# Kernel optimization log

Measured on AMD Instinct MI355X. Metric: run time of the kernel, lower is better.

The kernel has to match this reference:

```python
import jax, jax.numpy as jnp
import numpy as np

V, H, F, E, S, N, O = 50000, 1024, 4096, 8, 128, 4096, 2


def setup_inputs() -> dict:
    key = jax.random.key(0)
    ks = jax.random.split(key, 9)
    x = jax.random.randint(ks[0], (N, S), 0, V)
    emb = jax.random.normal(ks[1], (V, H), dtype=jnp.float32) * 0.02
    emb = emb.at[0].set(0.0)  # padding_idx=0
    Wg = jax.random.normal(ks[2], (H, E), dtype=jnp.float32) * 0.02
    W1 = jax.random.normal(ks[3], (E, H, F), dtype=jnp.float32) * 0.02
    b1 = jnp.zeros((E, F), dtype=jnp.float32)
    W2 = jax.random.normal(ks[4], (E, F, H), dtype=jnp.float32) * 0.02
    b2 = jnp.zeros((E, H), dtype=jnp.float32)
    Wfc = jax.random.normal(ks[5], (H, O), dtype=jnp.float32) * 0.02
    bfc = jnp.zeros((O,), dtype=jnp.float32)
    return {"x": x, "emb": emb, "Wg": Wg, "W1": W1, "b1": b1,
            "W2": W2, "b2": b2, "Wfc": Wfc, "bfc": bfc}


def reference(x, emb, Wg, W1, b1, W2, b2, Wfc, bfc):
    # embedding lookup + mean pool over sequence: [N, S, H] -> [N, H]
    h = emb[x].mean(axis=1)
    # top-1 gating (deepspeed MoE default k=1)
    gates = jax.nn.softmax(h @ Wg, axis=-1)              # [N, E]
    idx = jnp.argmax(gates, axis=-1)                      # [N]
    onehot = jax.nn.one_hot(idx, E, dtype=h.dtype)        # [N, E]
    combine = gates * onehot                              # [N, E] top-1 prob
    # dense-dispatch reference for grouped expert GEMMs (FFN: H->F->H, ReLU)
    h1 = jax.nn.relu(jnp.einsum('nh,ehf->nef', h, W1) + b1)  # [N, E, F]
    h2 = jnp.einsum('nef,efh->neh', h1, W2) + b2             # [N, E, H]
    moe = jnp.einsum('ne,neh->nh', combine, h2)              # [N, H]
    return jax.nn.log_softmax(moe @ Wfc + bfc, axis=1)       # [N, O]
```

## Files before the change

kernel.cpp:

```cpp
#include <hip/hip_runtime.h>
#include <stdint.h>

#define V_SZ 50000
#define H_DIM 1024
#define F_DIM 4096
#define E_NUM 8
#define S_LEN 128
#define N_TOK 4096
#define NPAD (N_TOK + E_NUM*128)
#define EMB_SCALE 16.0f

typedef unsigned short u16;
typedef unsigned int u32;
typedef unsigned char u8;
typedef short bf16x8 __attribute__((ext_vector_type(8)));
typedef float f32x4 __attribute__((ext_vector_type(4)));
typedef float f32x2 __attribute__((ext_vector_type(2)));

__device__ __forceinline__ u16 f2bf(float f) {
  u32 u = __builtin_bit_cast(u32, f);
  u += 0x7fffu + ((u >> 16) & 1u);
  return (u16)(u >> 16);
}
__device__ __forceinline__ u32 pack2(float a, float b) {
  return (u32)f2bf(a) | ((u32)f2bf(b) << 16);
}

__device__ __forceinline__ void gld_lds16(u16* lds, const u16* g) {
  __builtin_amdgcn_global_load_lds((const __attribute__((address_space(1))) void*)g,
                                   (__attribute__((address_space(3))) void*)lds,
                                   16, 0, 0);
}

__global__ void embconv_kernel(const float* __restrict__ emb, u8* __restrict__ embf8) {
  const size_t total = (size_t)V_SZ*H_DIM/8;
  const size_t stride = (size_t)gridDim.x*blockDim.x;
  for (size_t i = (size_t)blockIdx.x*blockDim.x + threadIdx.x; i < total; i += stride) {
    const float4 a = ((const float4*)emb)[i*2];
    const float4 b = ((const float4*)emb)[i*2+1];
    u32 w0, w1;
    w0 = __builtin_amdgcn_cvt_pk_fp8_f32(a.x*EMB_SCALE, a.y*EMB_SCALE, 0u, false);
    w0 = __builtin_amdgcn_cvt_pk_fp8_f32(a.z*EMB_SCALE, a.w*EMB_SCALE, w0, true);
    w1 = __builtin_amdgcn_cvt_pk_fp8_f32(b.x*EMB_SCALE, b.y*EMB_SCALE, 0u, false);
    w1 = __builtin_amdgcn_cvt_pk_fp8_f32(b.z*EMB_SCALE, b.w*EMB_SCALE, w1, true);
    ((uint2*)embf8)[i] = make_uint2(w0, w1);
  }
}

__global__ void poolgate_kernel(const int* __restrict__ x, const u8* __restrict__ embf8,
                                const float* __restrict__ Wg,
                                u16* __restrict__ hB, float* __restrict__ gate_val,
                                int* __restrict__ gate_idx, int* __restrict__ cnt) {
  __shared__ int sidx[S_LEN];
  __shared__ float wsum[4][8];
  const int n = blockIdx.x, t = threadIdx.x;
  if (t < S_LEN) sidx[t] = x[n*S_LEN + t];
  __syncthreads();
  float a0 = 0.f, a1 = 0.f, a2 = 0.f, a3 = 0.f;
  #pragma unroll 8
  for (int s = 0; s < S_LEN; ++s) {
    const u32 w = *(const u32*)(embf8 + (size_t)sidx[s]*H_DIM + t*4);
    const f32x2 lo = __builtin_amdgcn_cvt_pk_f32_fp8(w, false);
    const f32x2 hi = __builtin_amdgcn_cvt_pk_f32_fp8(w, true);
    a0 += lo[0]; a1 += lo[1]; a2 += hi[0]; a3 += hi[1];
  }
  const float sc = 1.0f/((float)S_LEN * EMB_SCALE);
  a0 *= sc; a1 *= sc; a2 *= sc; a3 *= sc;
  uint2 pk; pk.x = pack2(a0, a1); pk.y = pack2(a2, a3);
  *(uint2*)&hB[(size_t)n*H_DIM + t*4] = pk;
  float lg[E_NUM];
  #pragma unroll
  for (int e = 0; e < E_NUM; ++e) lg[e] = 0.f;
  const float hv[4] = {a0, a1, a2, a3};
  #pragma unroll
  for (int j = 0; j < 4; ++j) {
    const float4* w4 = (const float4*)(Wg + (size_t)(t*4+j)*E_NUM);
    const float4 wa = w4[0], wb = w4[1];
    lg[0] += hv[j]*wa.x; lg[1] += hv[j]*wa.y; lg[2] += hv[j]*wa.z; lg[3] += hv[j]*wa.w;
    lg[4] += hv[j]*wb.x; lg[5] += hv[j]*wb.y; lg[6] += hv[j]*wb.z; lg[7] += hv[j]*wb.w;
  }
  #pragma unroll
  for (int m = 32; m >= 1; m >>= 1) {
    #pragma unroll
    for (int e = 0; e < E_NUM; ++e) lg[e] += __shfl_xor(lg[e], m);
  }
  if ((t & 63) == 0) {
    #pragma unroll
    for (int e = 0; e < E_NUM; ++e) wsum[t >> 6][e] = lg[e];
  }
  __syncthreads();
  if (t == 0) {
    float l[E_NUM];
    #pragma unroll
    for (int e = 0; e < E_NUM; ++e)
      l[e] = wsum[0][e] + wsum[1][e] + wsum[2][e] + wsum[3][e];
    float mx = l[0]; int im = 0;
    #pragma unroll
    for (int e = 1; e < E_NUM; ++e) if (l[e] > mx) { mx = l[e]; im = e; }
    float s = 0.f;
    #pragma unroll
    for (int e = 0; e < E_NUM; ++e) s += expf(l[e] - mx);
    gate_val[n] = 1.0f / s;
    gate_idx[n] = im;
    atomicAdd(&cnt[im], 1);
  }
}

__global__ void offsets_kernel(const int* __restrict__ cnt, int* __restrict__ pad_off) {
  int o = 0;
  for (int e = 0; e < E_NUM; ++e) {
    pad_off[e] = o;
    o += ((cnt[e] + 127) >> 7) << 7;
  }
  pad_off[E_NUM] = o;
}

__global__ void scatterconv_kernel(const u16* __restrict__ hB, const int* __restrict__ gate_idx,
                                   const int* __restrict__ pad_off, int* __restrict__ cursor,
                                   int* __restrict__ perm, u16* __restrict__ Hg) {
  __shared__ int srow;
  const int n = blockIdx.x, t = threadIdx.x;
  if (t == 0) {
    const int e = gate_idx[n];
    const int pos = atomicAdd(&cursor[e], 1);
    const int row = pad_off[e] + pos;
    perm[row] = n;
    srow = row;
  }
  __syncthreads();
  const int row = srow;
  const uint4 v = *(const uint4*)(hB + (size_t)n*H_DIM + t*8);
  *(uint4*)&Hg[(size_t)row*H_DIM + t*8] = v;
}

template<int C, int RPER>
__global__ void ct_kernel(const float* __restrict__ in, u16* __restrict__ out) {
  __shared__ float tile[64][65];
  const int c0 = blockIdx.x*64, r0 = blockIdx.y*64;
  const int t = threadIdx.x;
  const int cq = t & 15, rr = t >> 4;
  #pragma unroll
  for (int p = 0; p < 4; ++p) {
    const int row = p*16 + rr;
    float4 v = ((const float4*)(in + (size_t)(r0+row)*C + c0))[cq];
    tile[row][cq*4+0] = v.x; tile[row][cq*4+1] = v.y;
    tile[row][cq*4+2] = v.z; tile[row][cq*4+3] = v.w;
  }
  __syncthreads();
  const int slot = t & 7, nn = t >> 3;
  const int e = r0 / RPER, rl0 = r0 % RPER;
  u16* outE = out + (size_t)e*C*RPER;
  #pragma unroll
  for (int p = 0; p < 2; ++p) {
    const int nc = p*32 + nn;
    uint4 q;
    q.x = pack2(tile[slot*8+0][nc], tile[slot*8+1][nc]);
    q.y = pack2(tile[slot*8+2][nc], tile[slot*8+3][nc]);
    q.z = pack2(tile[slot*8+4][nc], tile[slot*8+5][nc]);
    q.w = pack2(tile[slot*8+6][nc], tile[slot*8+7][nc]);
    *(uint4*)&outE[(size_t)(c0+nc)*RPER + rl0 + slot*8] = q;
  }
}

template<int KTOT, int EPI>
__launch_bounds__(256, 2)
__global__ void gemm_kernel(const u16* __restrict__ A, const u16* __restrict__ B,
                            const float* __restrict__ bias,
                            const float* __restrict__ gate_val,
                            const int* __restrict__ perm,
                            const int* __restrict__ pad_off,
                            const int* __restrict__ cnt,
                            u16* __restrict__ out_bf, float* __restrict__ out_f) {
  constexpr int MD = (EPI == 1) ? F_DIM : H_DIM;
  const int e = blockIdx.z;
  const int seg0 = pad_off[e], seg1 = pad_off[e+1];
  if ((int)blockIdx.y*128 >= seg1 - seg0) return;
  const int t0 = seg0 + blockIdx.y*128;
  const int f0 = blockIdx.x*128;
  const u16* Ae = A + (size_t)e*MD*KTOT;

  __shared__ u16 As[128*64];
  __shared__ u16 Bs[128*64];

  const int tid = threadIdx.x;
  const int lane = tid & 63, wave = tid >> 6;
  const int wm = wave >> 1, wn = wave & 1;

  f32x4 acc[4][4];
  #pragma unroll
  for (int i = 0; i < 4; ++i)
    #pragma unroll
    for (int j = 0; j < 4; ++j) acc[i][j] = (f32x4){0.f, 0.f, 0.f, 0.f};

  const int rsub = lane >> 3, slot = lane & 7;
  const int csw = slot ^ rsub;
  const int fr = lane & 15, fg = lane >> 4;

  for (int kk = 0; kk < KTOT; kk += 64) {
    __syncthreads();
    #pragma unroll
    for (int i = 0; i < 4; ++i) {
      const int chunk = wave*4 + i;
      const int r = chunk*8 + rsub;
      gld_lds16(&As[chunk*512], Ae + (size_t)(f0 + r)*KTOT + kk + csw*8);
      gld_lds16(&Bs[chunk*512], B  + (size_t)(t0 + r)*KTOT + kk + csw*8);
    }
    __syncthreads();
    #pragma unroll
    for (int kh = 0; kh < 2; ++kh) {
      bf16x8 av[4], bv[4];
      #pragma unroll
      for (int mi = 0; mi < 4; ++mi) {
        const int ra = wm*64 + mi*16 + fr;
        const int sa = (kh*4 + fg) ^ (ra & 7);
        av[mi] = *(const bf16x8*)&As[ra*64 + sa*8];
      }
      #pragma unroll
      for (int ni = 0; ni < 4; ++ni) {
        const int rb = wn*64 + ni*16 + fr;
        const int sb = (kh*4 + fg) ^ (rb & 7);
        bv[ni] = *(const bf16x8*)&Bs[rb*64 + sb*8];
      }
      #pragma unroll
      for (int mi = 0; mi < 4; ++mi)
        #pragma unroll
        for (int ni = 0; ni < 4; ++ni)
          acc[mi][ni] = __builtin_amdgcn_mfma_f32_16x16x32_bf16(av[mi], bv[ni], acc[mi][ni], 0, 0, 0);
    }
  }

  #pragma unroll
  for (int mi = 0; mi < 4; ++mi) {
    const int gm0 = f0 + wm*64 + mi*16 + fg*4;
    #pragma unroll
    for (int ni = 0; ni < 4; ++ni) {
      const int gn = wn*64 + ni*16 + fr;
      if constexpr (EPI == 1) {
        const float* bp = bias + (size_t)e*MD + gm0;
        const float v0 = fmaxf(acc[mi][ni][0] + bp[0], 0.f);
        const float v1 = fmaxf(acc[mi][ni][1] + bp[1], 0.f);
        const float v2 = fmaxf(acc[mi][ni][2] + bp[2], 0.f);
        const float v3 = fmaxf(acc[mi][ni][3] + bp[3], 0.f);
        uint2 pk; pk.x = pack2(v0, v1); pk.y = pack2(v2, v3);
        *(uint2*)&out_bf[(size_t)(t0 + gn)*F_DIM + gm0] = pk;
      } else {
        const int local = blockIdx.y*128 + gn;
        if (local < cnt[e]) {
          const int tok = perm[t0 + gn];
          const float g = gate_val[tok];
          const float* bp = bias + (size_t)e*MD + gm0;
          f32x4 v;
          v[0] = (acc[mi][ni][0] + bp[0]) * g;
          v[1] = (acc[mi][ni][1] + bp[1]) * g;
          v[2] = (acc[mi][ni][2] + bp[2]) * g;
          v[3] = (acc[mi][ni][3] + bp[3]) * g;
          *(f32x4*)&out_f[(size_t)tok*H_DIM + gm0] = v;
        }
      }
    }
  }
}

__global__ void final_kernel(const float* __restrict__ moe, const float* __restrict__ Wfc,
                             const float* __restrict__ bfc, float* __restrict__ out) {
  const int n = blockIdx.x, l = threadIdx.x;
  const float4* m4 = (const float4*)(moe + (size_t)n*H_DIM);
  const float2* w2 = (const float2*)Wfc;
  float a0 = 0.f, a1 = 0.f;
  #pragma unroll
  for (int j = 0; j < H_DIM/256; ++j) {
    const int i4 = j*64 + l;
    const float4 v = m4[i4];
    const int hh = i4*4;
    const float2 q0 = w2[hh], q1 = w2[hh+1], q2 = w2[hh+2], q3 = w2[hh+3];
    a0 += v.x*q0.x + v.y*q1.x + v.z*q2.x + v.w*q3.x;
    a1 += v.x*q0.y + v.y*q1.y + v.z*q2.y + v.w*q3.y;
  }
  #pragma unroll
  for (int m = 32; m >= 1; m >>= 1) { a0 += __shfl_xor(a0, m); a1 += __shfl_xor(a1, m); }
  if (l == 0) {
    const float l0 = a0 + bfc[0], l1 = a1 + bfc[1];
    const float mx = fmaxf(l0, l1);
    const float lse = mx + logf(expf(l0 - mx) + expf(l1 - mx));
    out[(size_t)n*2 + 0] = l0 - lse;
    out[(size_t)n*2 + 1] = l1 - lse;
  }
}

extern "C" void kernel_launch(void* const* d_in, const int* in_sizes, int n_in,
                              void* d_out, int out_size, void* d_ws, size_t ws_size,
                              hipStream_t stream) {
  const int*   x   = (const int*)  d_in[0];
  const float* emb = (const float*)d_in[1];
  const float* Wg  = (const float*)d_in[2];
  const float* W1  = (const float*)d_in[3];
  const float* b1  = (const float*)d_in[4];
  const float* W2  = (const float*)d_in[5];
  const float* b2  = (const float*)d_in[6];
  const float* Wfc = (const float*)d_in[7];
  const float* bfc = (const float*)d_in[8];
  float* out = (float*)d_out;

  char* p = (char*)d_ws;
  size_t off = 0;
  auto alloc = [&](size_t bytes) {
    void* r = p + off;
    off = (off + bytes + 255) & ~(size_t)255;
    return r;
  };
  u16*   hB       = (u16*)  alloc((size_t)N_TOK*H_DIM*2);
  float* moe      = (float*)alloc((size_t)N_TOK*H_DIM*4);
  float* gate_val = (float*)alloc((size_t)N_TOK*4);
  int*   gate_idx = (int*)  alloc((size_t)N_TOK*4);
  int*   perm     = (int*)  alloc((size_t)NPAD*4);
  int*   meta     = (int*)  alloc(256);
  int* cnt = meta; int* cursor = meta + 8; int* pad_off = meta + 16;
  u16* Hg  = (u16*)alloc((size_t)NPAD*H_DIM*2);
  u16* H1  = (u16*)alloc((size_t)NPAD*F_DIM*2);
  char* uni = (char*)alloc((size_t)E_NUM*F_DIM*H_DIM*2*2);
  u8*  embf8 = (u8*)uni;
  u16* W1T   = (u16*)uni;
  u16* W2T   = W1T + (size_t)E_NUM*F_DIM*H_DIM;

  hipMemsetAsync(meta, 0, 256, stream);
  embconv_kernel<<<4096, 256, 0, stream>>>(emb, embf8);
  poolgate_kernel<<<N_TOK, 256, 0, stream>>>(x, embf8, Wg, hB, gate_val, gate_idx, cnt);
  offsets_kernel<<<1, 1, 0, stream>>>(cnt, pad_off);
  scatterconv_kernel<<<N_TOK, 128, 0, stream>>>(hB, gate_idx, pad_off, cursor, perm, Hg);
  ct_kernel<F_DIM, H_DIM><<<dim3(F_DIM/64, E_NUM*H_DIM/64), 256, 0, stream>>>(W1, W1T);
  ct_kernel<H_DIM, F_DIM><<<dim3(H_DIM/64, E_NUM*F_DIM/64), 256, 0, stream>>>(W2, W2T);
  gemm_kernel<H_DIM, 1><<<dim3(F_DIM/128, 32, E_NUM), 256, 0, stream>>>(
      W1T, Hg, b1, nullptr, nullptr, pad_off, cnt, H1, nullptr);
  gemm_kernel<F_DIM, 2><<<dim3(H_DIM/128, 32, E_NUM), 256, 0, stream>>>(
      W2T, H1, b2, gate_val, perm, pad_off, cnt, nullptr, moe);
  final_kernel<<<N_TOK, 64, 0, stream>>>(moe, Wfc, bfc, out);
}
```

Baseline: 805.5 us.

## Split-K the second expert GEMM and reduce partial planes in final kernel

The down-projection GEMM now splits its K=4096 reduction into 4 chunks, one per extra grid-z slice. Each slice writes raw fp32 partial sums to its own plane, reusing the transposed-weight workspace that the first GEMM no longer needs. The final kernel sums the four planes, adds the expert bias b2 and applies the gate weight before the Wfc projection. This raises the number of active blocks, which was limited by roughly 4 token tiles per expert. The cost is extra global traffic to write and re-read the partial planes.

```diff
diff --git a/kernel.cpp b/kernel.cpp
--- a/kernel.cpp
+++ b/kernel.cpp
@@ -9,6 +9,7 @@
 #define N_TOK 4096
 #define NPAD (N_TOK + E_NUM*128)
 #define EMB_SCALE 16.0f
+#define SK2 4
 
 typedef unsigned short u16;
 typedef unsigned int u32;
@@ -162,17 +163,17 @@
   }
 }
 
-template<int KTOT, int EPI>
+template<int KTOT, int EPI, int SK>
 __launch_bounds__(256, 2)
 __global__ void gemm_kernel(const u16* __restrict__ A, const u16* __restrict__ B,
                             const float* __restrict__ bias,
-                            const float* __restrict__ gate_val,
                             const int* __restrict__ perm,
                             const int* __restrict__ pad_off,
                             const int* __restrict__ cnt,
                             u16* __restrict__ out_bf, float* __restrict__ out_f) {
   constexpr int MD = (EPI == 1) ? F_DIM : H_DIM;
-  const int e = blockIdx.z;
+  const int e  = blockIdx.z / SK;
+  const int kc = blockIdx.z % SK;
   const int seg0 = pad_off[e], seg1 = pad_off[e+1];
   if ((int)blockIdx.y*128 >= seg1 - seg0) return;
   const int t0 = seg0 + blockIdx.y*128;
@@ -196,7 +197,8 @@
   const int csw = slot ^ rsub;
   const int fr = lane & 15, fg = lane >> 4;
 
-  for (int kk = 0; kk < KTOT; kk += 64) {
+  const int kbeg = kc*(KTOT/SK), kend = kbeg + KTOT/SK;
+  for (int kk = kbeg; kk < kend; kk += 64) {
     __syncthreads();
     #pragma unroll
     for (int i = 0; i < 4; ++i) {
@@ -247,34 +249,44 @@
         const int local = blockIdx.y*128 + gn;
         if (local < cnt[e]) {
           const int tok = perm[t0 + gn];
-          const float g = gate_val[tok];
-          const float* bp = bias + (size_t)e*MD + gm0;
-          f32x4 v;
-          v[0] = (acc[mi][ni][0] + bp[0]) * g;
-          v[1] = (acc[mi][ni][1] + bp[1]) * g;
-          v[2] = (acc[mi][ni][2] + bp[2]) * g;
-          v[3] = (acc[mi][ni][3] + bp[3]) * g;
-          *(f32x4*)&out_f[(size_t)tok*H_DIM + gm0] = v;
+          float* plane = out_f + (size_t)kc*N_TOK*H_DIM;
+          *(f32x4*)&plane[(size_t)tok*H_DIM + gm0] = acc[mi][ni];
         }
       }
     }
   }
 }
 
-__global__ void final_kernel(const float* __restrict__ moe, const float* __restrict__ Wfc,
+__global__ void final_kernel(const float* __restrict__ planes,
+                             const float* __restrict__ b2,
+                             const int* __restrict__ gate_idx,
+                             const float* __restrict__ gate_val,
+                             const float* __restrict__ Wfc,
                              const float* __restrict__ bfc, float* __restrict__ out) {
   const int n = blockIdx.x, l = threadIdx.x;
-  const float4* m4 = (const float4*)(moe + (size_t)n*H_DIM);
+  const int e = gate_idx[n];
+  const float g = gate_val[n];
+  const size_t pstride = (size_t)N_TOK*H_DIM/4;
+  const float4* p0 = (const float4*)planes + (size_t)n*(H_DIM/4);
+  const float4* b24 = (const float4*)(b2 + (size_t)e*H_DIM);
   const float2* w2 = (const float2*)Wfc;
   float a0 = 0.f, a1 = 0.f;
   #pragma unroll
   for (int j = 0; j < H_DIM/256; ++j) {
     const int i4 = j*64 + l;
-    const float4 v = m4[i4];
+    const float4 q0 = p0[i4];
+    const float4 q1 = p0[i4 + pstride];
+    const float4 q2 = p0[i4 + 2*pstride];
+    const float4 q3 = p0[i4 + 3*pstride];
+    const float4 bb = b24[i4];
+    const float vx = (q0.x+q1.x+q2.x+q3.x + bb.x)*g;
+    const float vy = (q0.y+q1.y+q2.y+q3.y + bb.y)*g;
+    const float vz = (q0.z+q1.z+q2.z+q3.z + bb.z)*g;
+    const float vw = (q0.w+q1.w+q2.w+q3.w + bb.w)*g;
     const int hh = i4*4;
-    const float2 q0 = w2[hh], q1 = w2[hh+1], q2 = w2[hh+2], q3 = w2[hh+3];
-    a0 += v.x*q0.x + v.y*q1.x + v.z*q2.x + v.w*q3.x;
-    a1 += v.x*q0.y + v.y*q1.y + v.z*q2.y + v.w*q3.y;
+    const float2 r0 = w2[hh], r1 = w2[hh+1], r2 = w2[hh+2], r3 = w2[hh+3];
+    a0 += vx*r0.x + vy*r1.x + vz*r2.x + vw*r3.x;
+    a1 += vx*r0.y + vy*r1.y + vz*r2.y + vw*r3.y;
   }
   #pragma unroll
   for (int m = 32; m >= 1; m >>= 1) { a0 += __shfl_xor(a0, m); a1 += __shfl_xor(a1, m); }
@@ -309,7 +321,6 @@
     return r;
   };
   u16*   hB       = (u16*)  alloc((size_t)N_TOK*H_DIM*2);
-  float* moe      = (float*)alloc((size_t)N_TOK*H_DIM*4);
   float* gate_val = (float*)alloc((size_t)N_TOK*4);
   int*   gate_idx = (int*)  alloc((size_t)N_TOK*4);
   int*   perm     = (int*)  alloc((size_t)NPAD*4);
@@ -318,9 +329,10 @@
   u16* Hg  = (u16*)alloc((size_t)NPAD*H_DIM*2);
   u16* H1  = (u16*)alloc((size_t)NPAD*F_DIM*2);
   char* uni = (char*)alloc((size_t)E_NUM*F_DIM*H_DIM*2*2);
-  u8*  embf8 = (u8*)uni;
-  u16* W1T   = (u16*)uni;
-  u16* W2T   = W1T + (size_t)E_NUM*F_DIM*H_DIM;
+  u8*  embf8  = (u8*)uni;
+  u16* W1T    = (u16*)uni;
+  u16* W2T    = W1T + (size_t)E_NUM*F_DIM*H_DIM;
+  float* planes = (float*)uni;
 
   hipMemsetAsync(meta, 0, 256, stream);
   embconv_kernel<<<4096, 256, 0, stream>>>(emb, embf8);
@@ -329,9 +341,9 @@
   scatterconv_kernel<<<N_TOK, 128, 0, stream>>>(hB, gate_idx, pad_off, cursor, perm, Hg);
   ct_kernel<F_DIM, H_DIM><<<dim3(F_DIM/64, E_NUM*H_DIM/64), 256, 0, stream>>>(W1, W1T);
   ct_kernel<H_DIM, F_DIM><<<dim3(H_DIM/64, E_NUM*F_DIM/64), 256, 0, stream>>>(W2, W2T);
-  gemm_kernel<H_DIM, 1><<<dim3(F_DIM/128, 32, E_NUM), 256, 0, stream>>>(
-      W1T, Hg, b1, nullptr, nullptr, pad_off, cnt, H1, nullptr);
-  gemm_kernel<F_DIM, 2><<<dim3(H_DIM/128, 32, E_NUM), 256, 0, stream>>>(
-      W2T, H1, b2, gate_val, perm, pad_off, cnt, nullptr, moe);
-  final_kernel<<<N_TOK, 64, 0, stream>>>(moe, Wfc, bfc, out);
-}
+  gemm_kernel<H_DIM, 1, 1><<<dim3(F_DIM/128, 32, E_NUM), 256, 0, stream>>>(
+      W1T, Hg, b1, nullptr, pad_off, cnt, H1, nullptr);
+  gemm_kernel<F_DIM, 2, SK2><<<dim3(H_DIM/128, 32, E_NUM*SK2), 256, 0, stream>>>(
+      W2T, H1, nullptr, perm, pad_off, cnt, nullptr, planes);
+  final_kernel<<<N_TOK, 64, 0, stream>>>(planes, b2, gate_idx, gate_val, Wfc, bfc, out);
+}
```

Result: faster. 756.6 us (-6.1%).
